# Performance work log

Measured on AMD Instinct MI355X. Metric: run time of the kernel, lower is better.

## Reference

```python
import jax, jax.numpy as jnp
import numpy as np

K = 9                 # num_keypoints
NA = 1                # num_anchors
NC = 1                # num_classes
NB, NH, NW = 16, 76, 76
NUM_LABELS = 2 * K + 3
MAX_T = 50
COORD_SCALE = 1.0
OBJECT_SCALE = 5.0
NOOBJECT_SCALE = 0.1
SIL_THRESH = 0.6
DIST_THRESH = 30.0
IM_W, IM_H = 640.0, 480.0
PRETRAIN_EPOCHS = 15
SHARP = 2.0           # sharpness in corner_confidences


def corner_conf(gt, pr):
    """gt, pr: [..., K, 2] normalized corner coords -> mean per-keypoint confidence [...]."""
    scale = jnp.asarray([IM_W, IM_H], dtype=gt.dtype)
    d = (gt - pr) * scale
    dist = jnp.sqrt(jnp.sum(d * d, axis=-1))                       # [..., K] pixel distance
    c = (jnp.exp(SHARP * (1.0 - dist / DIST_THRESH)) - 1.0) / (np.exp(SHARP) - 1.0)
    c = jnp.where(dist < DIST_THRESH, c, 0.0)
    return jnp.mean(c, axis=-1)


def setup_inputs() -> dict:
    key = jax.random.key(0)
    k1, k2 = jax.random.split(key)
    output = jax.random.normal(k1, (NB, NA * (2 * K + 1 + NC), NH, NW), dtype=jnp.float32)
    target = jax.random.uniform(k2, (NB, MAX_T * NUM_LABELS), dtype=jnp.float32)
    return {"output": output, "target": target, "epoch": 20}


def reference(output, target, epoch):
    out = output.reshape(NB, NA, 2 * K + 1 + NC, NH, NW)
    xs = out[:, :, 0:2 * K:2]                                      # [NB,NA,K,NH,NW]
    ys = out[:, :, 1:2 * K:2]
    xs = jnp.concatenate([jax.nn.sigmoid(xs[:, :, :1]), xs[:, :, 1:]], axis=2)  # sigmoid only kp0
    ys = jnp.concatenate([jax.nn.sigmoid(ys[:, :, :1]), ys[:, :, 1:]], axis=2)
    conf = jax.nn.sigmoid(out[:, :, 2 * K])                        # [NB,NA,NH,NW]

    # ---- predicted corners (detached, as in torch: x[i].data) ----
    xd = jax.lax.stop_gradient(xs)
    yd = jax.lax.stop_gradient(ys)
    grid_x = jnp.arange(NW, dtype=jnp.float32)
    grid_y = jnp.arange(NH, dtype=jnp.float32)
    px = (xd + grid_x[None, None, None, None, :]) / NW
    py = (yd + grid_y[None, None, None, :, None]) / NH
    pred = jnp.stack([px, py], axis=-1)                            # [NB,NA,K,NH,NW,2]
    pred = pred.transpose(0, 1, 3, 4, 2, 5).reshape(NB, NA * NH * NW, K, 2)

    # ---- ground-truth parsing ----
    tgt = jax.lax.stop_gradient(target).reshape(NB, MAX_T, NUM_LABELS)
    gt = tgt[:, :, 1:1 + 2 * K].reshape(NB, MAX_T, K, 2)           # normalized corners
    # loop breaks at first t with target[...,1]==0 -> prefix validity
    valid = jnp.cumprod((tgt[:, :, 1] != 0).astype(jnp.int32), axis=1).astype(bool)  # [NB,MAX_T]

    # ---- phase 1: silent-threshold conf mask ----
    confs = corner_conf(gt[:, :, None], pred[:, None])             # [NB,MAX_T,nAnchors]
    confs = jnp.where(valid[:, :, None], confs, 0.0)
    cur_confs = jnp.max(confs, axis=1)                             # running max, init 0 (confs>=0)
    conf_mask = jnp.where(cur_confs > SIL_THRESH, 0.0, NOOBJECT_SCALE).reshape(NB, NA, NH, NW)

    # ---- phase 2: per-GT assignment (best_n = 0) ----
    gx_all = gt[..., 0] * NW                                       # [NB,MAX_T,K]
    gy_all = gt[..., 1] * NH
    gi0 = gx_all[:, :, 0].astype(jnp.int32)                        # centroid cell
    gj0 = gy_all[:, :, 0].astype(jnp.int32)
    b_idx = jnp.broadcast_to(jnp.arange(NB)[:, None], (NB, MAX_T))
    gi = jnp.where(valid, gi0, NW)                                 # OOB index -> dropped scatter
    gj = jnp.where(valid, gj0, NH)
    a0 = jnp.zeros_like(gi)

    coord_mask = jnp.zeros((NB, NA, NH, NW)).at[b_idx, a0, gj, gi].set(1.0, mode='drop')
    conf_mask = conf_mask.at[b_idx, a0, gj, gi].set(OBJECT_SCALE, mode='drop')

    tx_vals = gx_all - gi0[..., None].astype(jnp.float32)          # [NB,MAX_T,K]
    ty_vals = gy_all - gj0[..., None].astype(jnp.float32)
    txs = jnp.zeros((NB, NA, NH, NW, K)).at[b_idx, a0, gj, gi].set(tx_vals, mode='drop')
    tys = jnp.zeros((NB, NA, NH, NW, K)).at[b_idx, a0, gj, gi].set(ty_vals, mode='drop')

    cell = jnp.clip(gj0 * NW + gi0, 0, NH * NW - 1)                # anchor-0 cell index
    pred_cells = pred.reshape(NB, NA, NH * NW, K, 2)[b_idx, 0, cell]  # [NB,MAX_T,K,2]
    tconf_vals = corner_conf(gt, pred_cells)                       # [NB,MAX_T]
    tconf = jnp.zeros((NB, NA, NH, NW)).at[b_idx, a0, gj, gi].set(tconf_vals, mode='drop')

    # ---- losses ----
    m = coord_mask[:, :, None]                                     # broadcast over K
    txs_t = jnp.moveaxis(txs, -1, 2)                               # [NB,NA,K,NH,NW]
    tys_t = jnp.moveaxis(tys, -1, 2)
    loss_x = COORD_SCALE * 0.5 * jnp.sum((xs * m - txs_t * m) ** 2)
    loss_y = COORD_SCALE * 0.5 * jnp.sum((ys * m - tys_t * m) ** 2)
    cm = jnp.sqrt(conf_mask)
    loss_conf = 0.5 * jnp.sum((conf * cm - tconf * cm) ** 2)
    if epoch > PRETRAIN_EPOCHS:
        loss = loss_x + loss_y + loss_conf
    else:
        loss = loss_x + loss_y
    return loss
```

## Files before the change

kernel.cpp:

```cpp
#include <hip/hip_runtime.h>
#include <math.h>

#define KPT 9
#define NB 16
#define NH 76
#define NW 76
#define MAX_T 50
#define NCH 20
#define NUM_LABELS 21
#define CELLS (NH*NW)
#define IM_W 640.0f
#define IM_H 480.0f
#define SX (IM_W/(float)NW)
#define SY (IM_H/(float)NH)
#define DIST_THRESH 30.0f
#define D2_THRESH (DIST_THRESH*DIST_THRESH)
#define SIL_THRESH 0.6f
#define OBJECT_SCALE 5.0f
#define NOOBJECT_SCALE 0.1f
#define PRETRAIN_EPOCHS 15
#define E2M1 6.3890560989306495f
#define CNORM (1.0f/(E2M1*9.0f))
#define CURMAX_BREAK (SIL_THRESH * E2M1 * 9.0f)
#define CNT_MIN 6

#define TSPLIT 4
#define CPB 64

__device__ __forceinline__ float sigmoidf_(float x) {
    return 1.0f / (1.0f + __expf(-x));
}

__global__ void zero_out_kernel(float* d_out) {
    d_out[0] = 0.0f;
}

__launch_bounds__(256)
__global__ void region_loss_kernel(const float* __restrict__ output,
                                   const float* __restrict__ target,
                                   const int* __restrict__ epoch_p,
                                   float* __restrict__ d_out)
{
    const int tid  = threadIdx.x;
    const int wave = tid >> 6;
    const int cl   = tid & 63;
    const int b    = blockIdx.y;
    const int cell = blockIdx.x * CPB + cl;
    const bool live = (cell < CELLS);

    __shared__ float2 s_gt[MAX_T][KPT];
    __shared__ float2 s_txy[MAX_T][KPT];
    __shared__ float  s_tconf[MAX_T];
    __shared__ int    s_cell[MAX_T];
    __shared__ int    s_nvalid;
    __shared__ float  s_sil[TSPLIT][CPB];
    __shared__ int    s_winp[TSPLIT][CPB];

    const float* tgb = target + (size_t)b * MAX_T * NUM_LABELS;

    if (tid < 64) {
        float v1 = (tid < MAX_T) ? tgb[tid * NUM_LABELS + 1] : 1.0f;
        unsigned long long zm = __ballot(v1 == 0.0f);
        if (tid == 0) {
            int fz = (zm == 0ULL) ? MAX_T : (__ffsll((long long)zm) - 1);
            s_nvalid = fz < MAX_T ? fz : MAX_T;
        }
    }

    if (tid < MAX_T) {
        const float* row = tgb + tid * NUM_LABELS;
        float gx0 = row[1] * (float)NW;
        float gy0 = row[2] * (float)NH;
        int gi0 = (int)gx0;
        int gj0 = (int)gy0;
        int cellt = gj0 * NW + gi0;
        int cellc = min(max(cellt, 0), CELLS - 1);
        int hc = cellc / NW, wc = cellc % NW;
        const float* ob = output + (size_t)b * NCH * CELLS + cellc;
        float csum = 0.0f;
        #pragma unroll
        for (int k = 0; k < KPT; ++k) {
            float gxk = row[1 + 2*k];
            float gyk = row[2 + 2*k];
            float gxp = gxk * IM_W;
            float gyp = gyk * IM_H;
            s_gt[tid][k]  = make_float2(gxp, gyp);
            s_txy[tid][k] = make_float2(gxk * (float)NW - (float)gi0,
                                        gyk * (float)NH - (float)gj0);
            float xo = ob[(2*k) * CELLS];
            float yo = ob[(2*k + 1) * CELLS];
            if (k == 0) { xo = sigmoidf_(xo); yo = sigmoidf_(yo); }
            float dx = gxp - (xo + (float)wc) * SX;
            float dy = gyp - (yo + (float)hc) * SY;
            float d2 = dx*dx + dy*dy;
            if (d2 < D2_THRESH) {
                csum += __expf(2.0f - sqrtf(d2) * (2.0f / DIST_THRESH)) - 1.0f;
            }
        }
        s_tconf[tid] = csum * CNORM;
        s_cell[tid] = (gi0 >= 0 && gi0 < NW && gj0 >= 0 && gj0 < NH) ? cellt : -1;
    }
    __syncthreads();

    const int nv = s_nvalid;

    float pxs[KPT], pys[KPT];
    float sil = 0.0f;
    int   win = -1;
    if (live) {
        const int h = cell / NW;
        const int w = cell - h * NW;
        const float* ob = output + (size_t)b * NCH * CELLS + cell;
        #pragma unroll
        for (int k = 0; k < KPT; ++k) {
            float xo = ob[(2*k) * CELLS];
            float yo = ob[(2*k + 1) * CELLS];
            if (k == 0) { xo = sigmoidf_(xo); yo = sigmoidf_(yo); }
            pxs[k] = (xo + (float)w) * SX;
            pys[k] = (yo + (float)h) * SY;
        }
        for (int t = wave; t < nv; t += TSPLIT) {
            int cnt = 0;
            #pragma unroll
            for (int k = 0; k < KPT; ++k) {
                float2 g = s_gt[t][k];
                float dx = g.x - pxs[k];
                float dy = g.y - pys[k];
                float d2 = __builtin_fmaf(dx, dx, dy*dy);
                cnt += (d2 < D2_THRESH) ? 1 : 0;
            }
            if (cnt >= CNT_MIN) {
                float csum = 0.0f;
                #pragma unroll
                for (int k = 0; k < KPT; ++k) {
                    float2 g = s_gt[t][k];
                    float dx = g.x - pxs[k];
                    float dy = g.y - pys[k];
                    float d2 = __builtin_fmaf(dx, dx, dy*dy);
                    if (d2 < D2_THRESH)
                        csum += __expf(2.0f - sqrtf(d2) * (2.0f / DIST_THRESH)) - 1.0f;
                }
                if (csum > CURMAX_BREAK) sil = 1.0f;
            }
            if (s_cell[t] == cell) win = t;
        }
    }
    s_sil[wave][cl]  = sil;
    s_winp[wave][cl] = win;
    __syncthreads();

    float contrib = 0.0f;
    if (wave == 0 && live) {
        float sl = fmaxf(fmaxf(s_sil[0][cl], s_sil[1][cl]),
                         fmaxf(s_sil[2][cl], s_sil[3][cl]));
        int wn = max(max(s_winp[0][cl], s_winp[1][cl]),
                     max(s_winp[2][cl], s_winp[3][cl]));
        const int h = cell / NW;
        const int w = cell - h * NW;
        const float* ob = output + (size_t)b * NCH * CELLS + cell;
        const float conf = sigmoidf_(ob[2*KPT * CELLS]);

        float cmask, tconf;
        if (wn >= 0) {
            cmask = OBJECT_SCALE;
            tconf = s_tconf[wn];
            #pragma unroll
            for (int k = 0; k < KPT; ++k) {
                float xo = pxs[k] * (1.0f/SX) - (float)w;
                float yo = pys[k] * (1.0f/SY) - (float)h;
                float2 txy = s_txy[wn][k];
                float dxv = xo - txy.x;
                float dyv = yo - txy.y;
                contrib += 0.5f * (dxv*dxv + dyv*dyv);
            }
        } else {
            cmask = (sl > 0.0f) ? 0.0f : NOOBJECT_SCALE;
            tconf = 0.0f;
        }
        if (epoch_p[0] > PRETRAIN_EPOCHS) {
            float d = conf - tconf;
            contrib += 0.5f * cmask * d * d;
        }
    }

    if (wave == 0) {
        #pragma unroll
        for (int off = 32; off > 0; off >>= 1)
            contrib += __shfl_down(contrib, off);
        if (cl == 0) atomicAdd(d_out, contrib);
    }
}

extern "C" void kernel_launch(void* const* d_in, const int* in_sizes, int n_in,
                              void* d_out, int out_size, void* d_ws, size_t ws_size,
                              hipStream_t stream) {
    const float* output = (const float*)d_in[0];
    const float* target = (const float*)d_in[1];
    const int*   epoch  = (const int*)d_in[2];
    float* out = (float*)d_out;

    zero_out_kernel<<<1, 1, 0, stream>>>(out);

    dim3 grid((CELLS + CPB - 1) / CPB, NB);
    region_loss_kernel<<<grid, 256, 0, stream>>>(output, target, epoch, out);
}
```

Baseline: 37.88 us.

## Split targets across eight waves, vectorize GT loads, scatter winners via shared atomics

Doubles the number of waves per block that share the target loop, so each wave handles fewer targets per cell. Ground-truth corners are packed into float4 rows, letting the per-target distance check issue wide LDS reads. The per-cell winner is now found once by a shared-memory atomicMax scatter from the target threads, which removes the per-iteration cell comparison and the cross-wave winner reduction. The cost is an extra barrier and larger blocks. Each block also reloads the per-cell keypoint outputs in more waves, which adds redundant global reads.

```diff
diff --git a/kernel.cpp b/kernel.cpp
--- a/kernel.cpp
+++ b/kernel.cpp
@@ -24,8 +24,9 @@
 #define CURMAX_BREAK (SIL_THRESH * E2M1 * 9.0f)
 #define CNT_MIN 6
 
-#define TSPLIT 4
+#define TSPLIT 8
 #define CPB 64
+#define NTHREADS (TSPLIT*64)
 
 __device__ __forceinline__ float sigmoidf_(float x) {
     return 1.0f / (1.0f + __expf(-x));
@@ -35,7 +36,7 @@
     d_out[0] = 0.0f;
 }
 
-__launch_bounds__(256)
+__launch_bounds__(NTHREADS)
 __global__ void region_loss_kernel(const float* __restrict__ output,
                                    const float* __restrict__ target,
                                    const int* __restrict__ epoch_p,
@@ -48,13 +49,12 @@
     const int cell = blockIdx.x * CPB + cl;
     const bool live = (cell < CELLS);
 
-    __shared__ float2 s_gt[MAX_T][KPT];
+    __shared__ float4 s_gt4[MAX_T][5];
     __shared__ float2 s_txy[MAX_T][KPT];
     __shared__ float  s_tconf[MAX_T];
-    __shared__ int    s_cell[MAX_T];
     __shared__ int    s_nvalid;
+    __shared__ int    s_win[CPB];
     __shared__ float  s_sil[TSPLIT][CPB];
-    __shared__ int    s_winp[TSPLIT][CPB];
 
     const float* tgb = target + (size_t)b * MAX_T * NUM_LABELS;
 
@@ -65,7 +65,9 @@
             int fz = (zm == 0ULL) ? MAX_T : (__ffsll((long long)zm) - 1);
             s_nvalid = fz < MAX_T ? fz : MAX_T;
         }
-    }
+        s_win[tid] = -1;
+    }
+    __syncthreads();
 
     if (tid < MAX_T) {
         const float* row = tgb + tid * NUM_LABELS;
@@ -77,6 +79,7 @@
         int cellc = min(max(cellt, 0), CELLS - 1);
         int hc = cellc / NW, wc = cellc % NW;
         const float* ob = output + (size_t)b * NCH * CELLS + cellc;
+        float* gdst = (float*)&s_gt4[tid][0];
         float csum = 0.0f;
         #pragma unroll
         for (int k = 0; k < KPT; ++k) {
@@ -84,7 +87,8 @@
             float gyk = row[2 + 2*k];
             float gxp = gxk * IM_W;
             float gyp = gyk * IM_H;
-            s_gt[tid][k]  = make_float2(gxp, gyp);
+            gdst[2*k]   = gxp;
+            gdst[2*k+1] = gyp;
             s_txy[tid][k] = make_float2(gxk * (float)NW - (float)gi0,
                                         gyk * (float)NH - (float)gj0);
             float xo = ob[(2*k) * CELLS];
@@ -97,8 +101,12 @@
                 csum += __expf(2.0f - sqrtf(d2) * (2.0f / DIST_THRESH)) - 1.0f;
             }
         }
+        gdst[18] = 1e18f; gdst[19] = 1e18f;
         s_tconf[tid] = csum * CNORM;
-        s_cell[tid] = (gi0 >= 0 && gi0 < NW && gj0 >= 0 && gj0 < NH) ? cellt : -1;
+        bool scatter_ok = (gi0 >= 0 && gi0 < NW && gj0 >= 0 && gj0 < NH) &&
+                          (tid < s_nvalid);
+        int c = cellt - blockIdx.x * CPB;
+        if (scatter_ok && c >= 0 && c < CPB) atomicMax(&s_win[c], tid);
     }
     __syncthreads();
 
@@ -106,7 +114,6 @@
 
     float pxs[KPT], pys[KPT];
     float sil = 0.0f;
-    int   win = -1;
     if (live) {
         const int h = cell / NW;
         const int w = cell - h * NW;
@@ -120,41 +127,47 @@
             pys[k] = (yo + (float)h) * SY;
         }
         for (int t = wave; t < nv; t += TSPLIT) {
+            float4 q0 = s_gt4[t][0];
+            float4 q1 = s_gt4[t][1];
+            float4 q2 = s_gt4[t][2];
+            float4 q3 = s_gt4[t][3];
+            float4 q4 = s_gt4[t][4];
             int cnt = 0;
-            #pragma unroll
-            for (int k = 0; k < KPT; ++k) {
-                float2 g = s_gt[t][k];
-                float dx = g.x - pxs[k];
-                float dy = g.y - pys[k];
-                float d2 = __builtin_fmaf(dx, dx, dy*dy);
-                cnt += (d2 < D2_THRESH) ? 1 : 0;
-            }
+            #define KP(gx, gy, k) { \
+                float dx = (gx) - pxs[k]; \
+                float dy = (gy) - pys[k]; \
+                float d2 = __builtin_fmaf(dx, dx, dy*dy); \
+                cnt += (d2 < D2_THRESH) ? 1 : 0; }
+            KP(q0.x, q0.y, 0) KP(q0.z, q0.w, 1)
+            KP(q1.x, q1.y, 2) KP(q1.z, q1.w, 3)
+            KP(q2.x, q2.y, 4) KP(q2.z, q2.w, 5)
+            KP(q3.x, q3.y, 6) KP(q3.z, q3.w, 7)
+            KP(q4.x, q4.y, 8)
+            #undef KP
             if (cnt >= CNT_MIN) {
+                const float* gq = (const float*)&s_gt4[t][0];
                 float csum = 0.0f;
                 #pragma unroll
                 for (int k = 0; k < KPT; ++k) {
-                    float2 g = s_gt[t][k];
-                    float dx = g.x - pxs[k];
-                    float dy = g.y - pys[k];
+                    float dx = gq[2*k]   - pxs[k];
+                    float dy = gq[2*k+1] - pys[k];
                     float d2 = __builtin_fmaf(dx, dx, dy*dy);
                     if (d2 < D2_THRESH)
                         csum += __expf(2.0f - sqrtf(d2) * (2.0f / DIST_THRESH)) - 1.0f;
                 }
                 if (csum > CURMAX_BREAK) sil = 1.0f;
             }
-            if (s_cell[t] == cell) win = t;
-        }
-    }
-    s_sil[wave][cl]  = sil;
-    s_winp[wave][cl] = win;
+        }
+    }
+    s_sil[wave][cl] = sil;
     __syncthreads();
 
     float contrib = 0.0f;
     if (wave == 0 && live) {
-        float sl = fmaxf(fmaxf(s_sil[0][cl], s_sil[1][cl]),
-                         fmaxf(s_sil[2][cl], s_sil[3][cl]));
-        int wn = max(max(s_winp[0][cl], s_winp[1][cl]),
-                     max(s_winp[2][cl], s_winp[3][cl]));
+        float sl = 0.0f;
+        #pragma unroll
+        for (int wv = 0; wv < TSPLIT; ++wv) sl = fmaxf(sl, s_sil[wv][cl]);
+        const int wn = s_win[cl];
         const int h = cell / NW;
         const int w = cell - h * NW;
         const float* ob = output + (size_t)b * NCH * CELLS + cell;
@@ -202,5 +215,5 @@
     zero_out_kernel<<<1, 1, 0, stream>>>(out);
 
     dim3 grid((CELLS + CPB - 1) / CPB, NB);
-    region_loss_kernel<<<grid, 256, 0, stream>>>(output, target, epoch, out);
-}
+    region_loss_kernel<<<grid, NTHREADS, 0, stream>>>(output, target, epoch, out);
+}
```

Result: faster. 35.51 us (-6.3%).
